# Optimization experiments

Hardware: AMD Instinct MI355X
Metric: run time of the kernel (lower is better)

## Reference

```python
import jax, jax.numpy as jnp
import numpy as np

B, S, D, H = 2, 2048, 1024, 16
HD = D // H

def setup_inputs() -> dict:
    key = jax.random.key(0)
    ks = jax.random.split(key, 5)
    x = jax.random.normal(ks[0], (B, S, D), dtype=jnp.float32)
    scale = float(np.sqrt(6.0 / (D + D)))  # xavier_uniform bound
    def xavier(k):
        return jax.random.uniform(k, (D, D), dtype=jnp.float32, minval=-scale, maxval=scale)
    WQ, WK, WV, WO = xavier(ks[1]), xavier(ks[2]), xavier(ks[3]), xavier(ks[4])
    # causal mask, 1 = valid, 0 = masked, shape (B, 1, S_q, S_k)
    mask = jnp.broadcast_to(jnp.tril(jnp.ones((S, S), dtype=jnp.int32)), (B, 1, S, S))
    return {"x": x, "WQ": WQ, "WK": WK, "WV": WV, "WO": WO, "mask": mask}

def reference(x, WQ, WK, WV, WO, mask):
    b, s, d = x.shape
    # projections and head split: (B, H, S, HD)
    def split_heads(t):
        return t.reshape(b, s, H, HD).transpose(0, 2, 1, 3)
    q = split_heads(x @ WQ)
    k = split_heads(x @ WK)
    v = split_heads(x @ WV)
    scores = jnp.einsum('bhqd,bhkd->bhqk', q, k) / jnp.sqrt(jnp.float32(HD))
    neg = jnp.finfo(scores.dtype).min
    scores = jnp.where(mask == 0, neg, scores)
    attn = jax.nn.softmax(scores, axis=-1)
    out = jnp.einsum('bhqk,bhkd->bhqd', attn, v)  # (B, H, S, HD)
    out = out.transpose(0, 2, 1, 3).reshape(b, s, d)
    return out @ WO
```

## Files before the change

### kernel.cpp

```cpp
#include <hip/hip_runtime.h>
#include <hip/hip_bf16.h>


typedef __attribute__((ext_vector_type(8))) short short8;
typedef __attribute__((ext_vector_type(4))) float floatx4;
typedef __attribute__((ext_vector_type(4))) unsigned short ushort4v;
typedef __attribute__((ext_vector_type(2))) unsigned int uint2v;

#define GLDS16(gp, lp) __builtin_amdgcn_global_load_lds( \
    (const __attribute__((address_space(1))) void*)(gp), \
    (__attribute__((address_space(3))) void*)(lp), 16, 0, 0)

#define EXP2F(x) __builtin_amdgcn_exp2f(x)
#define NEG_INF (-__builtin_inff())

__device__ __forceinline__ unsigned short f2bf(float f) {
  unsigned int u = __builtin_bit_cast(unsigned int, f);
  return (unsigned short)((u + 0x7fffu + ((u >> 16) & 1u)) >> 16);
}
__device__ __forceinline__ float bf2f(unsigned short h) {
  unsigned int u = ((unsigned int)h) << 16;
  return __builtin_bit_cast(float, u);
}
__device__ __forceinline__ unsigned int pack2bf(float a, float b) {
  unsigned int ua = (__builtin_bit_cast(unsigned int, a) + 0x8000u) >> 16;
  unsigned int ub = (__builtin_bit_cast(unsigned int, b) + 0x8000u) & 0xFFFF0000u;
  return ua | ub;
}
__device__ __forceinline__ floatx4 mfma16(short8 a, short8 b, floatx4 c) {
  return __builtin_amdgcn_mfma_f32_16x16x32_bf16(a, b, c, 0, 0, 0);
}

__global__ void k_convert_x(const float* __restrict__ x, unsigned short* __restrict__ xb) {
  int i = (blockIdx.x * 256 + threadIdx.x) * 4;
  ushort4v o;
  o.x = f2bf(x[i + 0]);
  o.y = f2bf(x[i + 1]);
  o.z = f2bf(x[i + 2]);
  o.w = f2bf(x[i + 3]);
  *(ushort4v*)(xb + i) = o;
}

__global__ void k_transpose_w(const float* __restrict__ WQ, const float* __restrict__ WK,
                              const float* __restrict__ WV, const float* __restrict__ WO,
                              unsigned short* __restrict__ wtq, unsigned short* __restrict__ wto) {
  __shared__ float tile[32][33];
  const float* W = (blockIdx.z == 0) ? WQ : (blockIdx.z == 1) ? WK : (blockIdx.z == 2) ? WV : WO;
  unsigned short* dst = (blockIdx.z < 3) ? (wtq + (size_t)blockIdx.z * 1024 * 1024) : wto;
  int tx = threadIdx.x & 31, ty = threadIdx.x >> 5;
  int bx = blockIdx.x, by = blockIdx.y;
#pragma unroll
  for (int j = 0; j < 4; ++j)
    tile[ty + j * 8][tx] = W[(size_t)(by * 32 + ty + j * 8) * 1024 + bx * 32 + tx];
  __syncthreads();
#pragma unroll
  for (int j = 0; j < 4; ++j)
    dst[(size_t)(bx * 32 + ty + j * 8) * 1024 + by * 32 + tx] = f2bf(tile[tx][ty + j * 8]);
}

template <int MODE>
__global__ __launch_bounds__(256, 2) void k_gemm(
    const unsigned short* __restrict__ A, const unsigned short* __restrict__ BT,
    float* __restrict__ Cf, unsigned short* __restrict__ Qp,
    unsigned short* __restrict__ Kp, unsigned short* __restrict__ Vt, int K) {
  __shared__ __align__(16) unsigned short smem[128 * 136];
  unsigned short* lA = smem;
  unsigned short* lB = smem + 128 * 64;
  const int tid = threadIdx.x;
  const int wave = tid >> 6, lane = tid & 63;
  const int wm = wave & 1, wn = wave >> 1;
  const int m0 = blockIdx.x * 128, n0 = blockIdx.y * 128;
  const int l15 = lane & 15, l16 = lane >> 4;
  const int r8 = lane >> 3, c8 = lane & 7;
  const int gchunk = (c8 ^ r8) << 3;

  floatx4 acc[4][4] = {};
  for (int k0 = 0; k0 < K; k0 += 64) {
    __syncthreads();
#pragma unroll
    for (int i = 0; i < 4; ++i) {
      int seg = wave * 4 + i;
      int row = seg * 8 + r8;
      GLDS16(A + (size_t)(m0 + row) * K + k0 + gchunk, lA + seg * 512);
      GLDS16(BT + (size_t)(n0 + row) * K + k0 + gchunk, lB + seg * 512);
    }
    __syncthreads();
#pragma unroll
    for (int ks = 0; ks < 2; ++ks) {
      short8 af[4], bfr[4];
#pragma unroll
      for (int t = 0; t < 4; ++t) {
        int m = wm * 64 + t * 16 + l15;
        int cl = ks * 4 + l16;
        af[t] = *(const short8*)(lA + m * 64 + ((cl ^ (m & 7)) << 3));
        int n = wn * 64 + t * 16 + l15;
        bfr[t] = *(const short8*)(lB + n * 64 + ((cl ^ (n & 7)) << 3));
      }
#pragma unroll
      for (int mt = 0; mt < 4; ++mt)
#pragma unroll
        for (int nt = 0; nt < 4; ++nt)
          acc[mt][nt] = mfma16(af[mt], bfr[nt], acc[mt][nt]);
    }
  }
  const int sel = n0 >> 10;
  if (MODE == 1) {
#pragma unroll
    for (int mt = 0; mt < 4; ++mt)
#pragma unroll
      for (int nt = 0; nt < 4; ++nt)
#pragma unroll
        for (int r = 0; r < 4; ++r) {
          int m = m0 + wm * 64 + mt * 16 + l16 * 4 + r;
          int n = n0 + wn * 64 + nt * 16 + l15;
          Cf[(size_t)m * 1024 + n] = acc[mt][nt][r];
        }
  } else if (sel < 2) {
    unsigned short* dst = (sel == 0) ? Qp : Kp;
#pragma unroll
    for (int mt = 0; mt < 4; ++mt)
#pragma unroll
      for (int nt = 0; nt < 4; ++nt)
#pragma unroll
        for (int r = 0; r < 4; ++r) {
          int m = m0 + wm * 64 + mt * 16 + l16 * 4 + r;
          int n = n0 + wn * 64 + nt * 16 + l15;
          int b = m >> 11, s = m & 2047;
          int nn = n & 1023, h = nn >> 6, hd = nn & 63;
          dst[((size_t)((b * 16 + h) * 2048 + s) << 6) + hd] = f2bf(acc[mt][nt][r]);
        }
  } else {
    __syncthreads();
#pragma unroll
    for (int mt = 0; mt < 4; ++mt)
#pragma unroll
      for (int nt = 0; nt < 4; ++nt)
#pragma unroll
        for (int r = 0; r < 4; ++r) {
          int nl = wn * 64 + nt * 16 + l15;
          int ml = wm * 64 + mt * 16 + l16 * 4 + r;
          smem[nl * 136 + ml] = f2bf(acc[mt][nt][r]);
        }
    __syncthreads();
    const int b = m0 >> 11, s0 = m0 & 2047;
    const int h0 = (n0 - 2048) >> 6;
#pragma unroll
    for (int it = 0; it < 8; ++it) {
      int nl = it * 16 + (tid >> 4);
      int sc = (tid & 15) * 8;
      short8 v = *(const short8*)(smem + nl * 136 + sc);
      int hh = h0 + (nl >> 6), hd = nl & 63;
      *(short8*)(Vt + ((size_t)(b * 16 + hh) * 64 + hd) * 2048 + s0 + sc) = v;
    }
  }
}

__global__ __launch_bounds__(256, 2) void k_attn(
    const unsigned short* __restrict__ Qp, const unsigned short* __restrict__ Kp,
    const unsigned short* __restrict__ Vt, unsigned short* __restrict__ O) {
  __shared__ __align__(16) unsigned short pbuf[4][32 * 64];
  const int tid = threadIdx.x, wave = tid >> 6, lane = tid & 63;
  const int job = blockIdx.x * 4 + wave;
  const int g = job >> 5;
  const int strip = (g < 32) ? (63 - g) : (g - 32);
  const int bh = job & 31;
  const int l15 = lane & 15, l16 = lane >> 4;
  const int R0 = strip * 32;
  const size_t base = (size_t)bh << 17;
  unsigned short* pb = &pbuf[wave][0];

  const float qscale = 0.125f * 1.44269504088896f;
  short8 qf[2][2];
#pragma unroll
  for (int mt = 0; mt < 2; ++mt)
#pragma unroll
    for (int ks = 0; ks < 2; ++ks) {
      short8 v = *(const short8*)(Qp + base + (size_t)(R0 + mt * 16 + l15) * 64 + ks * 32 + l16 * 8);
#pragma unroll
      for (int j = 0; j < 8; ++j) {
        float f = bf2f((unsigned short)v[j]) * qscale;
        v[j] = (short)f2bf(f);
      }
      qf[mt][ks] = v;
    }
  short8 onesv;
#pragma unroll
  for (int j = 0; j < 8; ++j) onesv[j] = (short)0x3F80;

  floatx4 oacc[4][2] = {};
  floatx4 lacc[2] = {};

#define LOADK(KT, DST) \
  { _Pragma("unroll") for (int i_ = 0; i_ < 8; ++i_) \
      DST[i_] = *(const short8*)(Kp + base + \
          (size_t)((KT) * 64 + (i_ >> 1) * 16 + l15) * 64 + (i_ & 1) * 32 + l16 * 8); }

#define ATTN_STEP(KT, KC, KN) \
  { \
    int ktn_ = ((KT) + 1 < nkt) ? (KT) + 1 : (KT); \
    LOADK(ktn_, KN); \
    short8 vf_[8]; \
    _Pragma("unroll") for (int i_ = 0; i_ < 8; ++i_) \
      vf_[i_] = *(const short8*)(Vt + base + (size_t)((i_ >> 1) * 16 + l15) * 2048 + \
                                 (KT) * 64 + (i_ & 1) * 32 + l16 * 8); \
    floatx4 sacc_[2][4]; \
    _Pragma("unroll") for (int mt_ = 0; mt_ < 2; ++mt_) \
      _Pragma("unroll") for (int nt_ = 0; nt_ < 4; ++nt_) { \
        sacc_[mt_][nt_][0] = 0.f; sacc_[mt_][nt_][1] = 0.f; \
        sacc_[mt_][nt_][2] = 0.f; sacc_[mt_][nt_][3] = 0.f; \
      } \
    _Pragma("unroll") for (int ks_ = 0; ks_ < 2; ++ks_) \
      _Pragma("unroll") for (int mt_ = 0; mt_ < 2; ++mt_) \
        _Pragma("unroll") for (int nt_ = 0; nt_ < 4; ++nt_) \
          sacc_[mt_][nt_] = mfma16(KC[nt_ * 2 + ks_], qf[mt_][ks_], sacc_[mt_][nt_]); \
    if ((KT) * 64 + 63 > R0) { \
      _Pragma("unroll") for (int mt_ = 0; mt_ < 2; ++mt_) \
        _Pragma("unroll") for (int nt_ = 0; nt_ < 4; ++nt_) \
          _Pragma("unroll") for (int r_ = 0; r_ < 4; ++r_) { \
            int key_ = (KT) * 64 + nt_ * 16 + l16 * 4 + r_; \
            int qrow_ = R0 + mt_ * 16 + l15; \
            if (key_ > qrow_) sacc_[mt_][nt_][r_] = NEG_INF; \
          } \
    } \
    _Pragma("unroll") for (int mt_ = 0; mt_ < 2; ++mt_) \
      _Pragma("unroll") for (int nt_ = 0; nt_ < 4; ++nt_) { \
        uint2v pk_; \
        pk_.x = pack2bf(EXP2F(sacc_[mt_][nt_][0]), EXP2F(sacc_[mt_][nt_][1])); \
        pk_.y = pack2bf(EXP2F(sacc_[mt_][nt_][2]), EXP2F(sacc_[mt_][nt_][3])); \
        int q_ = mt_ * 16 + l15; \
        int ch_ = (nt_ * 4 + l16) ^ ((q_ & 7) << 1); \
        *(uint2v*)(pb + q_ * 64 + ch_ * 4) = pk_; \
      } \
    short8 pfr_[2][2]; \
    _Pragma("unroll") for (int mt_ = 0; mt_ < 2; ++mt_) \
      _Pragma("unroll") for (int ks_ = 0; ks_ < 2; ++ks_) { \
        int q_ = mt_ * 16 + l15; \
        int ch_ = (ks_ * 8 + l16 * 2) ^ ((q_ & 7) << 1); \
        pfr_[mt_][ks_] = *(const short8*)(pb + q_ * 64 + ch_ * 4); \
      } \
    _Pragma("unroll") for (int ks_ = 0; ks_ < 2; ++ks_) \
      _Pragma("unroll") for (int mt_ = 0; mt_ < 2; ++mt_) { \
        lacc[mt_] = mfma16(onesv, pfr_[mt_][ks_], lacc[mt_]); \
        _Pragma("unroll") for (int ht_ = 0; ht_ < 4; ++ht_) \
          oacc[ht_][mt_] = mfma16(vf_[ht_ * 2 + ks_], pfr_[mt_][ks_], oacc[ht_][mt_]); \
      } \
  }

  const int nkt = (R0 + 95) >> 6;
  short8 kA[8], kB[8];
  LOADK(0, kA);
  int kt = 0;
  while (true) {
    ATTN_STEP(kt, kA, kB);
    ++kt;
    if (kt >= nkt) break;
    ATTN_STEP(kt, kB, kA);
    ++kt;
    if (kt >= nkt) break;
  }
#undef ATTN_STEP
#undef LOADK

  const int b = bh >> 4, h = bh & 15;
  float inv[2];
#pragma unroll
  for (int mt = 0; mt < 2; ++mt) inv[mt] = 1.0f / lacc[mt][0];
#pragma unroll
  for (int ht = 0; ht < 4; ++ht)
#pragma unroll
    for (int mt = 0; mt < 2; ++mt) {
      int srow = R0 + mt * 16 + l15;
      uint2v pk;
      pk.x = pack2bf(oacc[ht][mt][0] * inv[mt], oacc[ht][mt][1] * inv[mt]);
      pk.y = pack2bf(oacc[ht][mt][2] * inv[mt], oacc[ht][mt][3] * inv[mt]);
      *(uint2v*)(O + (size_t)(b * 2048 + srow) * 1024 + h * 64 + ht * 16 + l16 * 4) = pk;
    }
}

extern "C" void kernel_launch(void* const* d_in, const int* in_sizes, int n_in,
                              void* d_out, int out_size, void* d_ws, size_t ws_size,
                              hipStream_t stream) {
  const float* x = (const float*)d_in[0];
  const float* WQ = (const float*)d_in[1];
  const float* WK = (const float*)d_in[2];
  const float* WV = (const float*)d_in[3];
  const float* WO = (const float*)d_in[4];
  float* out = (float*)d_out;
  char* ws = (char*)d_ws;
  unsigned short* xb = (unsigned short*)(ws);
  unsigned short* wtq = (unsigned short*)(ws + 8388608);
  unsigned short* wto = (unsigned short*)(ws + 14680064);
  unsigned short* Qp = (unsigned short*)(ws + 16777216);
  unsigned short* Kp = (unsigned short*)(ws + 25165824);
  unsigned short* Vt = (unsigned short*)(ws + 33554432);
  unsigned short* Ob = (unsigned short*)(ws + 41943040);

  k_convert_x<<<dim3(4096), dim3(256), 0, stream>>>(x, xb);
  k_transpose_w<<<dim3(32, 32, 4), dim3(256), 0, stream>>>(WQ, WK, WV, WO, wtq, wto);
  k_gemm<0><<<dim3(32, 24), dim3(256), 0, stream>>>(xb, wtq, (float*)nullptr, Qp, Kp, Vt, 1024);
  k_attn<<<dim3(512), dim3(256), 0, stream>>>(Qp, Kp, Vt, Ob);
  k_gemm<1><<<dim3(32, 8), dim3(256), 0, stream>>>(Ob, wto, out, (unsigned short*)nullptr,
                                                   (unsigned short*)nullptr,
                                                   (unsigned short*)nullptr, 1024);
}
```

Before: 217.5 us.

## Split attention KV tiles across wave pairs and stage Q/K stores via LDS

The attention kernel now assigns each query strip to a pair of waves that process alternating key tiles. Their partial output and row-sum accumulators are combined through shared memory before normalisation, and the grid is doubled with launch bounds raised to 4 blocks per CU. This is meant to shorten the long serial key loop per wave and raise occupancy, at the cost of extra LDS, a block-wide barrier and a reduction step. Separately, the Q/K projection epilogue now transposes through LDS so global stores are 16-byte vectorised rows instead of scattered 2-byte writes.

```diff
diff --git a/kernel.cpp b/kernel.cpp
--- a/kernel.cpp
+++ b/kernel.cpp
@@ -117,18 +117,28 @@
         }
   } else if (sel < 2) {
     unsigned short* dst = (sel == 0) ? Qp : Kp;
+    __syncthreads();
 #pragma unroll
     for (int mt = 0; mt < 4; ++mt)
 #pragma unroll
       for (int nt = 0; nt < 4; ++nt)
 #pragma unroll
         for (int r = 0; r < 4; ++r) {
-          int m = m0 + wm * 64 + mt * 16 + l16 * 4 + r;
-          int n = n0 + wn * 64 + nt * 16 + l15;
-          int b = m >> 11, s = m & 2047;
-          int nn = n & 1023, h = nn >> 6, hd = nn & 63;
-          dst[((size_t)((b * 16 + h) * 2048 + s) << 6) + hd] = f2bf(acc[mt][nt][r]);
+          int ml = wm * 64 + mt * 16 + l16 * 4 + r;
+          int nl = wn * 64 + nt * 16 + l15;
+          smem[ml * 136 + nl] = f2bf(acc[mt][nt][r]);
         }
+    __syncthreads();
+    const int b = m0 >> 11, s0 = m0 & 2047;
+    const int h0 = (n0 & 1023) >> 6;
+#pragma unroll
+    for (int it = 0; it < 8; ++it) {
+      int ml = it * 16 + (tid >> 4);
+      int c = (tid & 15) * 8;
+      short8 v = *(const short8*)(smem + ml * 136 + c);
+      int h = h0 + (c >> 6), hd = c & 63;
+      *(short8*)(dst + ((size_t)((b * 16 + h) * 2048 + s0 + ml) << 6) + hd) = v;
+    }
   } else {
     __syncthreads();
 #pragma unroll
@@ -155,12 +165,14 @@
   }
 }
 
-__global__ __launch_bounds__(256, 2) void k_attn(
+__global__ __launch_bounds__(256, 4) void k_attn(
     const unsigned short* __restrict__ Qp, const unsigned short* __restrict__ Kp,
     const unsigned short* __restrict__ Vt, unsigned short* __restrict__ O) {
   __shared__ __align__(16) unsigned short pbuf[4][32 * 64];
+  __shared__ __align__(16) float cbuf[2][64][36];
   const int tid = threadIdx.x, wave = tid >> 6, lane = tid & 63;
-  const int job = blockIdx.x * 4 + wave;
+  const int pair = wave >> 1, parity = wave & 1;
+  const int job = blockIdx.x * 2 + pair;
   const int g = job >> 5;
   const int strip = (g < 32) ? (63 - g) : (g - 32);
   const int bh = job & 31;
@@ -197,7 +209,7 @@
 
 #define ATTN_STEP(KT, KC, KN) \
   { \
-    int ktn_ = ((KT) + 1 < nkt) ? (KT) + 1 : (KT); \
+    int ktn_ = ((KT) + 2 < nkt) ? (KT) + 2 : (KT); \
     LOADK(ktn_, KN); \
     short8 vf_[8]; \
     _Pragma("unroll") for (int i_ = 0; i_ < 8; ++i_) \
@@ -248,33 +260,55 @@
 
   const int nkt = (R0 + 95) >> 6;
   short8 kA[8], kB[8];
-  LOADK(0, kA);
-  int kt = 0;
-  while (true) {
-    ATTN_STEP(kt, kA, kB);
-    ++kt;
-    if (kt >= nkt) break;
-    ATTN_STEP(kt, kB, kA);
-    ++kt;
-    if (kt >= nkt) break;
+  if (parity < nkt) {
+    LOADK(parity, kA);
+    int kt = parity;
+    while (true) {
+      ATTN_STEP(kt, kA, kB);
+      kt += 2;
+      if (kt >= nkt) break;
+      ATTN_STEP(kt, kB, kA);
+      kt += 2;
+      if (kt >= nkt) break;
+    }
   }
 #undef ATTN_STEP
 #undef LOADK
 
-  const int b = bh >> 4, h = bh & 15;
-  float inv[2];
-#pragma unroll
-  for (int mt = 0; mt < 2; ++mt) inv[mt] = 1.0f / lacc[mt][0];
-#pragma unroll
-  for (int ht = 0; ht < 4; ++ht)
-#pragma unroll
-    for (int mt = 0; mt < 2; ++mt) {
-      int srow = R0 + mt * 16 + l15;
-      uint2v pk;
-      pk.x = pack2bf(oacc[ht][mt][0] * inv[mt], oacc[ht][mt][1] * inv[mt]);
-      pk.y = pack2bf(oacc[ht][mt][2] * inv[mt], oacc[ht][mt][3] * inv[mt]);
-      *(uint2v*)(O + (size_t)(b * 2048 + srow) * 1024 + h * 64 + ht * 16 + l16 * 4) = pk;
-    }
+  if (parity == 1) {
+#pragma unroll
+    for (int ht = 0; ht < 4; ++ht)
+#pragma unroll
+      for (int mt = 0; mt < 2; ++mt)
+        *(floatx4*)&cbuf[pair][lane][(ht * 2 + mt) * 4] = oacc[ht][mt];
+    cbuf[pair][lane][32] = lacc[0][0];
+    cbuf[pair][lane][33] = lacc[1][0];
+  }
+  __syncthreads();
+  if (parity == 0) {
+#pragma unroll
+    for (int ht = 0; ht < 4; ++ht)
+#pragma unroll
+      for (int mt = 0; mt < 2; ++mt) {
+        floatx4 o2 = *(const floatx4*)&cbuf[pair][lane][(ht * 2 + mt) * 4];
+        oacc[ht][mt][0] += o2[0]; oacc[ht][mt][1] += o2[1];
+        oacc[ht][mt][2] += o2[2]; oacc[ht][mt][3] += o2[3];
+      }
+    float inv[2];
+    inv[0] = 1.0f / (lacc[0][0] + cbuf[pair][lane][32]);
+    inv[1] = 1.0f / (lacc[1][0] + cbuf[pair][lane][33]);
+    const int b = bh >> 4, h = bh & 15;
+#pragma unroll
+    for (int ht = 0; ht < 4; ++ht)
+#pragma unroll
+      for (int mt = 0; mt < 2; ++mt) {
+        int srow = R0 + mt * 16 + l15;
+        uint2v pk;
+        pk.x = pack2bf(oacc[ht][mt][0] * inv[mt], oacc[ht][mt][1] * inv[mt]);
+        pk.y = pack2bf(oacc[ht][mt][2] * inv[mt], oacc[ht][mt][3] * inv[mt]);
+        *(uint2v*)(O + (size_t)(b * 2048 + srow) * 1024 + h * 64 + ht * 16 + l16 * 4) = pk;
+      }
+  }
 }
 
 extern "C" void kernel_launch(void* const* d_in, const int* in_sizes, int n_in,
@@ -298,7 +332,7 @@
   k_convert_x<<<dim3(4096), dim3(256), 0, stream>>>(x, xb);
   k_transpose_w<<<dim3(32, 32, 4), dim3(256), 0, stream>>>(WQ, WK, WV, WO, wtq, wto);
   k_gemm<0><<<dim3(32, 24), dim3(256), 0, stream>>>(xb, wtq, (float*)nullptr, Qp, Kp, Vt, 1024);
-  k_attn<<<dim3(512), dim3(256), 0, stream>>>(Qp, Kp, Vt, Ob);
+  k_attn<<<dim3(1024), dim3(256), 0, stream>>>(Qp, Kp, Vt, Ob);
   k_gemm<1><<<dim3(32, 8), dim3(256), 0, stream>>>(Ob, wto, out, (unsigned short*)nullptr,
                                                    (unsigned short*)nullptr,
                                                    (unsigned short*)nullptr, 1024);
```

Result: slower. 384.9 us (+77.0%).
